# Kernel tuning notes

Measured on AMD Instinct MI355X. Metric: run time of the kernel, lower is better.

## Reference

```python
import jax, jax.numpy as jnp
import numpy as np
from jax import lax

B, H, W, C = 4, 1024, 1024, 16


def setup_inputs() -> dict:
    key = jax.random.key(0)
    k1, k2 = jax.random.split(key)
    feat = jax.random.normal(k1, (B, H, W, C), dtype=jnp.float32)
    mask = jax.random.randint(k2, (B, H, W), 0, 2).astype(bool)
    return {"feat": feat, "mask": mask}


def _sum_pool(f, m):
    """Minkowski sum pooling, kernel 3, stride 2, dilation 1, dim 2.

    Output coord c exists iff any input coord in {2c, 2c+1}^2 is occupied
    (floor(coord/2) strided coordinate map). Output feature at c sums input
    features at 2c + {-1,0,1}^2 (3x3 window centered on the strided coord).
    """
    f = f * m[..., None].astype(f.dtype)  # zero features at empty coords
    # 3x3 sum window, stride 2, pad 1 -> output spatial dims H//2, W//2
    out = lax.reduce_window(
        f, jnp.zeros((), f.dtype), lax.add,
        window_dimensions=(1, 3, 3, 1),
        window_strides=(1, 2, 2, 1),
        padding=((0, 0), (1, 1), (1, 1), (0, 0)),
    )
    b, h, w = m.shape
    m2 = m.reshape(b, h // 2, 2, w // 2, 2).any(axis=(2, 4))  # strided coord map
    out = out * m2[..., None].astype(out.dtype)  # keep only occupied outputs
    return out, m2


def reference(feat, mask):
    c1, m1 = _sum_pool(feat, mask)
    c2, m2 = _sum_pool(c1, m1)
    c3, m3 = _sum_pool(c2, m2)
    return (c2, c3)
```

## Files before the change

kernel.cpp:

```cpp
#include <hip/hip_runtime.h>


constexpr int Hh = 1024, Ww = 1024;
constexpr int TW3 = 16, TH3 = 8;
constexpr int NU = 4 * TW3 + 3;
constexpr int NV = 2 * TW3 + 1;
constexpr int NY = TW3;
constexpr int NTH = 320;
constexpr int NS = 4 * TH3 + 3;

#define BARRIER_LDS() asm volatile("s_waitcnt lgkmcnt(0)\ns_barrier" ::: "memory")

__device__ inline float4 add3(const float4& a, const float4& b, const float4& c) {
    return make_float4(a.x + b.x + c.x, a.y + b.y + c.y,
                       a.z + b.z + c.z, a.w + b.w + c.w);
}

__global__ __launch_bounds__(NTH) void fused3(
    const float* __restrict__ featp, const int* __restrict__ maskp,
    float4* __restrict__ c2o, float4* __restrict__ c3o)
{
    const int j = blockIdx.x;
    const int k = blockIdx.y;
    const int b = blockIdx.z;
    const int P0 = TW3 * j, Q0 = TH3 * k;
    const int F0 = 8 * P0 - 7;
    const int S0 = 4 * Q0 - 3;

    const int tid = threadIdx.x;
    const int c4 = tid & 3;
    const int u  = tid >> 2;
    const bool aAct = tid < NU * 4;
    const bool vAct = tid < NV * 4;
    const bool yAct = tid < NY * 4;

    __shared__ float4 c1m[2][NU][5];
    __shared__ float4 c2mS[NV][5];
    __shared__ unsigned char m1L[2][NU];
    __shared__ unsigned char m2L[NV];

    const float4* feat4 = reinterpret_cast<const float4*>(featp);
    const float4 z4 = make_float4(0.f, 0.f, 0.f, 0.f);

    auto ldMaskRow = [&](int t, int* mm) {
        mm[0] = mm[1] = mm[2] = 0;
        if (aAct && (unsigned)t < (unsigned)Hh) {
            const int base = (b * Hh + t) * Ww;
#pragma unroll
            for (int dw = 0; dw < 3; ++dw) {
                const int fc = F0 + 2 * u + dw;
                if ((unsigned)fc < (unsigned)Ww) mm[dw] = maskp[base + fc];
            }
        }
    };
    auto ldFeatRow = [&](int t, const int* mm, float4* ff) {
        ff[0] = ff[1] = ff[2] = z4;
        if (aAct && (unsigned)t < (unsigned)Hh) {
            const size_t base = (size_t)(b * Hh + t) * Ww;
#pragma unroll
            for (int dw = 0; dw < 3; ++dw) {
                if (mm[dw])
                    ff[dw] = feat4[(base + (F0 + 2 * u + dw)) * 4 + c4];
            }
        }
    };

    int   mA[6];
    float4 ffA[6];
    float4 h_prev;
    int   mp_cur;
    {
        int mP[3], m0[6];
        ldMaskRow(2 * S0 - 1, mP);
        ldMaskRow(2 * S0,     m0);
        ldMaskRow(2 * S0 + 1, m0 + 3);
        ldMaskRow(2 * S0 + 2, mA);
        ldMaskRow(2 * S0 + 3, mA + 3);
        float4 fP[3];
        ldFeatRow(2 * S0 - 1, mP, fP);
        ldFeatRow(2 * S0,     m0, ffA);
        ldFeatRow(2 * S0 + 1, m0 + 3, ffA + 3);
        h_prev = add3(fP[0], fP[1], fP[2]);
        mp_cur = m0[1] | m0[2] | m0[4] | m0[5];
    }

    float4 r2h0 = z4, r2h1 = z4;
    float4 r3h0 = z4, r3h1 = z4;
    int m2save = 0, m3save = 0;

    for (int i = 0; i < NS; ++i) {
        const int sb = i & 1;
        const float4 hc_e = add3(ffA[0], ffA[1], ffA[2]);
        const float4 hc_o = add3(ffA[3], ffA[4], ffA[5]);
        if (aAct) {
            float4 cv = z4;
            if (mp_cur) cv = add3(h_prev, hc_e, hc_o);
            c1m[sb][u][c4] = cv;
            if (c4 == 0) m1L[sb][u] = (unsigned char)(mp_cur ? 1 : 0);
        }
        const float4 hp_new = hc_o;
        const int mp_new = mA[1] | mA[2] | mA[4] | mA[5];
        const int t2 = 2 * (S0 + i) + 2;
        if (i + 1 < NS) {
            ldFeatRow(t2,     mA,     ffA);
            ldFeatRow(t2 + 1, mA + 3, ffA + 3);
        }
        if (i + 2 < NS) {
            ldMaskRow(t2 + 2, mA);
            ldMaskRow(t2 + 3, mA + 3);
        }
        BARRIER_LDS();
        float4 r2c = z4; int m2p = 0;
        if (vAct) {
            const float4 a0 = c1m[sb][2 * u + 0][c4];
            const float4 a1 = c1m[sb][2 * u + 1][c4];
            const float4 a2 = c1m[sb][2 * u + 2][c4];
            r2c = add3(a0, a1, a2);
            m2p = m1L[sb][2 * u + 1] | m1L[sb][2 * u + 2];
        }
        if ((i & 1) == 0) {
            const int r = 2 * Q0 - 2 + (i >> 1);
            if (vAct) {
                const int m2 = m2save | m2p;
                float4 c2v = z4;
                if (m2) c2v = add3(r2h0, r2h1, r2c);
                if (i >= 4 && u >= 1)
                    c2o[((size_t)((b * 256 + r) * 256 + (2 * P0 - 1 + u))) * 4 + c4] = c2v;
                c2mS[u][c4] = c2v;
                if (c4 == 0) m2L[u] = (unsigned char)(m2 ? 1 : 0);
            }
            BARRIER_LDS();
            float4 r3c = z4; int m3p = 0;
            if (yAct) {
                const float4 b0 = c2mS[2 * u + 0][c4];
                const float4 b1 = c2mS[2 * u + 1][c4];
                const float4 b2 = c2mS[2 * u + 2][c4];
                r3c = add3(b0, b1, b2);
                m3p = m2L[2 * u + 1] | m2L[2 * u + 2];
            }
            if ((i & 2) == 0) {
                m3save = m3p;
            } else if (yAct && i >= 6) {
                const int m3 = m3save | m3p;
                float4 c3v = z4;
                if (m3) c3v = add3(r3h0, r3h1, r3c);
                const int q = Q0 + ((i - 6) >> 2);
                c3o[((size_t)((b * 128 + q) * 128 + (P0 + u))) * 4 + c4] = c3v;
            }
            r3h0 = r3h1; r3h1 = r3c;
        } else {
            m2save = m2p;
        }
        r2h0 = r2h1; r2h1 = r2c;
        h_prev = hp_new; mp_cur = mp_new;
    }
}

extern "C" void kernel_launch(void* const* d_in, const int* in_sizes, int n_in,
                              void* d_out, int out_size, void* d_ws, size_t ws_size,
                              hipStream_t stream)
{
    const float* feat = (const float*)d_in[0];
    const int*   mask = (const int*)d_in[1];
    float4* c2 = (float4*)d_out;
    float4* c3 = c2 + (size_t)4 * 256 * 256 * 4;

    dim3 grid(Ww / (8 * TW3) , Hh / (8 * TH3) , 4);
    fused3<<<grid, NTH, 0, stream>>>(feat, mask, c2, c3);
}
```

Baseline: 60.83 us.

## Process two level-1 rows per iteration to halve barriers and deepen prefetch

The streaming loop now handles four input rows, that is two level-1 output rows, per iteration instead of two. Each iteration always computes a level-2 row and then a level-3 partial, so the odd and even phases are merged. Masks are prefetched one iteration further ahead using ping-pong register buffers, unrolled by two so the buffers can swap statically. This cuts the number of LDS barriers and loop iterations and gives more loads in flight, at the cost of higher register pressure (12 float4 feature registers plus 24 mask ints).

```diff
diff --git a/kernel.cpp b/kernel.cpp
--- a/kernel.cpp
+++ b/kernel.cpp
@@ -7,7 +7,7 @@
 constexpr int NV = 2 * TW3 + 1;
 constexpr int NY = TW3;
 constexpr int NTH = 320;
-constexpr int NS = 4 * TH3 + 3;
+constexpr int NQ = 2 * TH3 + 2;
 
 #define BARRIER_LDS() asm volatile("s_waitcnt lgkmcnt(0)\ns_barrier" ::: "memory")
 
@@ -25,7 +25,7 @@
     const int b = blockIdx.z;
     const int P0 = TW3 * j, Q0 = TH3 * k;
     const int F0 = 8 * P0 - 7;
-    const int S0 = 4 * Q0 - 3;
+    const int T0 = 8 * Q0 - 6;
 
     const int tid = threadIdx.x;
     const int c4 = tid & 3;
@@ -65,94 +65,113 @@
         }
     };
 
-    int   mA[6];
-    float4 ffA[6];
+    int mBufA[12], mBufB[12];
+    float4 ff[12];
     float4 h_prev;
-    int   mp_cur;
+    int mp0, mp1;
     {
-        int mP[3], m0[6];
-        ldMaskRow(2 * S0 - 1, mP);
-        ldMaskRow(2 * S0,     m0);
-        ldMaskRow(2 * S0 + 1, m0 + 3);
-        ldMaskRow(2 * S0 + 2, mA);
-        ldMaskRow(2 * S0 + 3, mA + 3);
+        int mP[3];
+        ldMaskRow(T0 - 1, mP);
+        ldMaskRow(T0 + 0, mBufA + 0);
+        ldMaskRow(T0 + 1, mBufA + 3);
+        ldMaskRow(T0 + 2, mBufA + 6);
+        ldMaskRow(T0 + 3, mBufA + 9);
+        ldMaskRow(T0 + 4, mBufB + 0);
+        ldMaskRow(T0 + 5, mBufB + 3);
+        ldMaskRow(T0 + 6, mBufB + 6);
+        ldMaskRow(T0 + 7, mBufB + 9);
         float4 fP[3];
-        ldFeatRow(2 * S0 - 1, mP, fP);
-        ldFeatRow(2 * S0,     m0, ffA);
-        ldFeatRow(2 * S0 + 1, m0 + 3, ffA + 3);
+        ldFeatRow(T0 - 1, mP, fP);
+        ldFeatRow(T0 + 0, mBufA + 0, ff + 0);
+        ldFeatRow(T0 + 1, mBufA + 3, ff + 3);
+        ldFeatRow(T0 + 2, mBufA + 6, ff + 6);
+        ldFeatRow(T0 + 3, mBufA + 9, ff + 9);
         h_prev = add3(fP[0], fP[1], fP[2]);
-        mp_cur = m0[1] | m0[2] | m0[4] | m0[5];
+        mp0 = mBufA[1] | mBufA[2] | mBufA[4]  | mBufA[5];
+        mp1 = mBufA[7] | mBufA[8] | mBufA[10] | mBufA[11];
     }
 
-    float4 r2h0 = z4, r2h1 = z4;
-    float4 r3h0 = z4, r3h1 = z4;
+    float4 r2p0 = z4, r2p1 = z4;
+    float4 r3p0 = z4, r3p1 = z4;
     int m2save = 0, m3save = 0;
 
-    for (int i = 0; i < NS; ++i) {
-        const int sb = i & 1;
-        const float4 hc_e = add3(ffA[0], ffA[1], ffA[2]);
-        const float4 hc_o = add3(ffA[3], ffA[4], ffA[5]);
+    auto body = [&](int i, int (&mCur)[12], int (&mNxt)[12]) {
+        const float4 hc0 = add3(ff[0], ff[1], ff[2]);
+        const float4 hc1 = add3(ff[3], ff[4], ff[5]);
+        const float4 hc2 = add3(ff[6], ff[7], ff[8]);
+        const float4 hc3 = add3(ff[9], ff[10], ff[11]);
         if (aAct) {
-            float4 cv = z4;
-            if (mp_cur) cv = add3(h_prev, hc_e, hc_o);
-            c1m[sb][u][c4] = cv;
-            if (c4 == 0) m1L[sb][u] = (unsigned char)(mp_cur ? 1 : 0);
+            float4 cv0 = z4, cv1 = z4;
+            if (mp0) cv0 = add3(h_prev, hc0, hc1);
+            if (mp1) cv1 = add3(hc1, hc2, hc3);
+            c1m[0][u][c4] = cv0;
+            c1m[1][u][c4] = cv1;
+            if (c4 == 0) {
+                m1L[0][u] = (unsigned char)(mp0 ? 1 : 0);
+                m1L[1][u] = (unsigned char)(mp1 ? 1 : 0);
+            }
         }
-        const float4 hp_new = hc_o;
-        const int mp_new = mA[1] | mA[2] | mA[4] | mA[5];
-        const int t2 = 2 * (S0 + i) + 2;
-        if (i + 1 < NS) {
-            ldFeatRow(t2,     mA,     ffA);
-            ldFeatRow(t2 + 1, mA + 3, ffA + 3);
+        h_prev = hc3;
+        mp0 = mCur[1] | mCur[2] | mCur[4]  | mCur[5];
+        mp1 = mCur[7] | mCur[8] | mCur[10] | mCur[11];
+        const int tq = T0 + 4 * (i + 1);
+        if (i + 1 < NQ) {
+            ldFeatRow(tq + 0, mCur + 0, ff + 0);
+            ldFeatRow(tq + 1, mCur + 3, ff + 3);
+            if (i + 1 != NQ - 1) {
+                ldFeatRow(tq + 2, mCur + 6, ff + 6);
+                ldFeatRow(tq + 3, mCur + 9, ff + 9);
+            }
         }
-        if (i + 2 < NS) {
-            ldMaskRow(t2 + 2, mA);
-            ldMaskRow(t2 + 3, mA + 3);
+        if (i + 2 < NQ) {
+            ldMaskRow(tq + 4, mNxt + 0);
+            ldMaskRow(tq + 5, mNxt + 3);
+            ldMaskRow(tq + 6, mNxt + 6);
+            ldMaskRow(tq + 7, mNxt + 9);
         }
         BARRIER_LDS();
-        float4 r2c = z4; int m2p = 0;
+        float4 r2c0 = z4, r2c1 = z4;
+        int m2p0 = 0, m2p1 = 0;
         if (vAct) {
-            const float4 a0 = c1m[sb][2 * u + 0][c4];
-            const float4 a1 = c1m[sb][2 * u + 1][c4];
-            const float4 a2 = c1m[sb][2 * u + 2][c4];
-            r2c = add3(a0, a1, a2);
-            m2p = m1L[sb][2 * u + 1] | m1L[sb][2 * u + 2];
+            r2c0 = add3(c1m[0][2 * u + 0][c4], c1m[0][2 * u + 1][c4], c1m[0][2 * u + 2][c4]);
+            r2c1 = add3(c1m[1][2 * u + 0][c4], c1m[1][2 * u + 1][c4], c1m[1][2 * u + 2][c4]);
+            m2p0 = m1L[0][2 * u + 1] | m1L[0][2 * u + 2];
+            m2p1 = m1L[1][2 * u + 1] | m1L[1][2 * u + 2];
+        }
+        if (vAct && i >= 1) {
+            const int m2 = m2save | m2p0;
+            float4 c2v = z4;
+            if (m2) c2v = add3(r2p0, r2p1, r2c0);
+            if (i >= 2 && u >= 1) {
+                const int r = 2 * Q0 - 2 + i;
+                c2o[((size_t)((b * 256 + r) * 256 + (2 * P0 - 1 + u))) * 4 + c4] = c2v;
+            }
+            c2mS[u][c4] = c2v;
+            if (c4 == 0) m2L[u] = (unsigned char)(m2 ? 1 : 0);
+        }
+        BARRIER_LDS();
+        float4 r3c = z4; int m3p = 0;
+        if (yAct && i >= 1) {
+            r3c = add3(c2mS[2 * u + 0][c4], c2mS[2 * u + 1][c4], c2mS[2 * u + 2][c4]);
+            m3p = m2L[2 * u + 1] | m2L[2 * u + 2];
         }
         if ((i & 1) == 0) {
-            const int r = 2 * Q0 - 2 + (i >> 1);
-            if (vAct) {
-                const int m2 = m2save | m2p;
-                float4 c2v = z4;
-                if (m2) c2v = add3(r2h0, r2h1, r2c);
-                if (i >= 4 && u >= 1)
-                    c2o[((size_t)((b * 256 + r) * 256 + (2 * P0 - 1 + u))) * 4 + c4] = c2v;
-                c2mS[u][c4] = c2v;
-                if (c4 == 0) m2L[u] = (unsigned char)(m2 ? 1 : 0);
-            }
-            BARRIER_LDS();
-            float4 r3c = z4; int m3p = 0;
-            if (yAct) {
-                const float4 b0 = c2mS[2 * u + 0][c4];
-                const float4 b1 = c2mS[2 * u + 1][c4];
-                const float4 b2 = c2mS[2 * u + 2][c4];
-                r3c = add3(b0, b1, b2);
-                m3p = m2L[2 * u + 1] | m2L[2 * u + 2];
-            }
-            if ((i & 2) == 0) {
-                m3save = m3p;
-            } else if (yAct && i >= 6) {
-                const int m3 = m3save | m3p;
-                float4 c3v = z4;
-                if (m3) c3v = add3(r3h0, r3h1, r3c);
-                const int q = Q0 + ((i - 6) >> 2);
-                c3o[((size_t)((b * 128 + q) * 128 + (P0 + u))) * 4 + c4] = c3v;
-            }
-            r3h0 = r3h1; r3h1 = r3c;
-        } else {
-            m2save = m2p;
+            m3save = m3p;
+        } else if (yAct && i >= 3) {
+            const int m3 = m3save | m3p;
+            float4 c3v = z4;
+            if (m3) c3v = add3(r3p0, r3p1, r3c);
+            const int q = Q0 + ((i - 3) >> 1);
+            c3o[((size_t)((b * 128 + q) * 128 + (P0 + u))) * 4 + c4] = c3v;
         }
-        r2h0 = r2h1; r2h1 = r2c;
-        h_prev = hp_new; mp_cur = mp_new;
+        r3p0 = r3p1; r3p1 = r3c;
+        r2p0 = r2c0; r2p1 = r2c1;
+        m2save = m2p1;
+    };
+
+    for (int ii = 0; ii < NQ; ii += 2) {
+        body(ii + 0, mBufB, mBufA);
+        body(ii + 1, mBufA, mBufB);
     }
 }
 
```

New measurement: 87.15 us. 43.3% more time.
